# Kernel tuning notes

Hardware: AMD Instinct MI355X
Metric: run time of the kernel (lower is better)

The kernel has to match this reference:

```python
import jax, jax.numpy as jnp
import numpy as np

N_E, E_DIM = 2048, 256
B, H, W = 32, 32, 32


def setup_inputs() -> dict:
    key = jax.random.key(0)
    k1, k2 = jax.random.split(key)
    z = jax.random.normal(k1, (B, E_DIM, H, W), dtype=jnp.float32)
    embedding = jax.random.normal(k2, (N_E, E_DIM), dtype=jnp.float32)
    return {"z": z, "embedding": embedding}


def reference(z, embedding):
    # z: [B, C, H, W] with C == e_dim; embedding: [n_e, e_dim]
    n_e, e_dim = embedding.shape
    b, c, h, w = z.shape
    z_nhwc = jnp.transpose(z, (0, 2, 3, 1))            # [B,H,W,C]
    z_flat = z_nhwc.reshape(-1, e_dim)                 # [L, D]
    # squared euclidean distance: ||z||^2 + ||e||^2 - 2 z.e^T
    d = (
        jnp.sum(z_flat * z_flat, axis=1, keepdims=True)
        + jnp.sum(embedding * embedding, axis=1)
        - 2.0 * jnp.einsum("ld,nd->ln", z_flat, embedding)
    )                                                  # [L, n_e]
    idx = jnp.argmin(d, axis=1)                        # [L]
    z_q = jnp.take(embedding, idx, axis=0).reshape(b, h, w, e_dim)
    # embed_ema=True -> commitment-only loss (codebook updated by EMA, not grads)
    loss = jnp.mean((jax.lax.stop_gradient(z_q) - z_nhwc) ** 2)
    # straight-through estimator
    z_q_st = z_nhwc + jax.lax.stop_gradient(z_q - z_nhwc)
    quantize = jnp.transpose(z_q_st, (0, 3, 1, 2))     # [B,C,H,W]
    # number of distinct codebook entries used (jit-safe via scatter-set)
    used = jnp.sum(jnp.zeros((n_e,), z.dtype).at[idx].set(1.0))
    index = idx.reshape(b, h, w)
    return quantize, loss, index, used
```

## Files before the change

kernel.cpp:

```cpp
#include <hip/hip_runtime.h>
#include <cfloat>

#define Dm 256
#define HW 1024
#define NE 2048
#define L_TOT 32768
#define QOFF 8388608
#define TAU 0.01f

typedef __attribute__((ext_vector_type(8))) short bf16x8;
typedef __attribute__((ext_vector_type(4))) float f32x4;
typedef const __attribute__((address_space(1))) unsigned int* as1_u32p;
typedef __attribute__((address_space(3))) unsigned int* as3_u32p;

#define GLL(gp, lp) __builtin_amdgcn_global_load_lds((as1_u32p)(gp), (as3_u32p)(lp), 16, 0, 0)

__device__ __forceinline__ unsigned short f2bf(float x) {
    unsigned u = __float_as_uint(x);
    unsigned r = (u + 0x7fffu + ((u >> 16) & 1u)) >> 16;
    return (unsigned short)r;
}
__device__ __forceinline__ float bf2f(unsigned short h) {
    return __uint_as_float(((unsigned)h) << 16);
}

__global__ void k_enorm(const float* __restrict__ emb, float* __restrict__ enorm) {
    int w = threadIdx.x >> 6, lane = threadIdx.x & 63;
    int n = blockIdx.x * 4 + w;
    const float4 v = *reinterpret_cast<const float4*>(emb + (size_t)n * Dm + lane * 4);
    double s = (double)v.x * v.x + (double)v.y * v.y + (double)v.z * v.z + (double)v.w * v.w;
    #pragma unroll
    for (int off = 32; off; off >>= 1) s += __shfl_xor(s, off);
    if (lane == 0) enorm[n] = (float)s;
}

__global__ __launch_bounds__(256) void k_split(
    const float* __restrict__ z, const float* __restrict__ emb,
    unsigned short* __restrict__ z_hi, unsigned short* __restrict__ z_lo,
    unsigned short* __restrict__ e_hi, unsigned short* __restrict__ e_lo,
    float* __restrict__ enorm, float* __restrict__ zn_part,
    float* __restrict__ used, int* __restrict__ flag_cnt)
{
    __shared__ unsigned short zh[32][260];
    __shared__ unsigned short zl[32][260];
    __shared__ double zsum[4];
    const int t = threadIdx.x;
    const int w = t >> 6, lane = t & 63;

    if (blockIdx.x >= 16 && blockIdx.x < 24) used[(blockIdx.x - 16) * 256 + t] = 0.f;
    if (blockIdx.x == 24 && t == 0) *flag_cnt = 0;

    if (w < 2) {
        int n = blockIdx.x * 2 + w;
        const float4 v = *reinterpret_cast<const float4*>(emb + (size_t)n * Dm + lane * 4);
        float vv[4] = { v.x, v.y, v.z, v.w };
        double s = (double)v.x * v.x + (double)v.y * v.y + (double)v.z * v.z + (double)v.w * v.w;
        #pragma unroll
        for (int off = 32; off; off >>= 1) s += __shfl_xor(s, off);
        if (lane == 0) enorm[n] = (float)s;
        ushort4 h4, l4;
        unsigned short* hp = (unsigned short*)&h4;
        unsigned short* lp = (unsigned short*)&l4;
        #pragma unroll
        for (int j = 0; j < 4; ++j) {
            unsigned short h = f2bf(vv[j]);
            hp[j] = h;
            lp[j] = f2bf(vv[j] - bf2f(h));
        }
        *reinterpret_cast<ushort4*>(e_hi + (size_t)n * Dm + lane * 4) = h4;
        *reinterpret_cast<ushort4*>(e_lo + (size_t)n * Dm + lane * 4) = l4;
    }

    const int b  = blockIdx.x >> 5;
    const int p0 = (blockIdx.x & 31) * 32;
    const int pp = t & 31, cb = t >> 5;
    const float* zb = z + (size_t)b * (Dm * HW) + p0 + pp;
    float zs = 0.f;
    for (int ci = 0; ci < 32; ++ci) {
        int c = ci * 8 + cb;
        float x = zb[(size_t)c * HW];
        zs = fmaf(x, x, zs);
        unsigned short h = f2bf(x);
        zh[pp][c] = h;
        zl[pp][c] = f2bf(x - bf2f(h));
    }
    double d = zs;
    #pragma unroll
    for (int off = 32; off; off >>= 1) d += __shfl_xor(d, off);
    if ((t & 63) == 0) zsum[w] = d;
    __syncthreads();
    if (t == 0) zn_part[blockIdx.x] = (float)(zsum[0] + zsum[1] + zsum[2] + zsum[3]);
    const int l0 = b * 1024 + p0;
    #pragma unroll
    for (int r = 0; r < 8; ++r) {
        int id = r * 256 + t;
        int row = id >> 6, ch = id & 63;
        *reinterpret_cast<ushort4*>(z_hi + (size_t)(l0 + row) * Dm + ch * 4) =
            *reinterpret_cast<ushort4*>(&zh[row][ch * 4]);
        *reinterpret_cast<ushort4*>(z_lo + (size_t)(l0 + row) * Dm + ch * 4) =
            *reinterpret_cast<ushort4*>(&zl[row][ch * 4]);
    }
}

__global__ __launch_bounds__(512, 4) void k_score2(
    const unsigned short* __restrict__ z_hi, const unsigned short* __restrict__ z_lo,
    const unsigned short* __restrict__ e_hi, const unsigned short* __restrict__ e_lo,
    const float* __restrict__ enorm,
    float* __restrict__ pd1, float* __restrict__ pd2, int* __restrict__ pi1)
{
    __shared__ unsigned short lds[2][2][128 * 64];

    const int t    = threadIdx.x;
    const int lane = t & 63, w = t >> 6;
    const int wm = w >> 2, wn = w & 3;
    const int c15 = lane & 15, g4 = lane >> 4;

    const int bx = blockIdx.x;
    const int wg = (bx & 7) * 64 + (bx >> 3);
    const int mi = wg >> 1, ni = wg & 1;
    const int l0 = mi * 128;
    const int nbase = ni * 1024;

    const int srow = t >> 3;
    const int chg  = (t & 7) ^ (srow & 7);
    const int aoff0 = (l0 + srow) * Dm + chg * 8;
    const int aoff1 = aoff0 + 64 * Dm;
    const int bbase = srow * Dm + chg * 8 + nbase * Dm;
    const int ld0 = t * 8, ld1 = t * 8 + 4096;

    auto stage = [&](int buf, const unsigned short* As, const unsigned short* Bs,
                     int ntoff, int k0) {
        GLL(As + aoff0 + k0,                 &lds[buf][0][ld0]);
        GLL(Bs + bbase + ntoff + k0,         &lds[buf][1][ld0]);
        GLL(As + aoff1 + k0,                 &lds[buf][0][ld1]);
        GLL(Bs + bbase + ntoff + 64 * Dm + k0, &lds[buf][1][ld1]);
    };

    float d1[4][4], d2[4][4]; int i1[4][4];
    #pragma unroll
    for (int m = 0; m < 4; ++m)
        #pragma unroll
        for (int r = 0; r < 4; ++r) { d1[m][r] = 3.4e38f; d2[m][r] = 3.4e38f; i1[m][r] = 0; }

    stage(0, z_hi, e_hi, 0, 0);
    __syncthreads();

    int cur = 0, it = 0;
    int pnt = 0, pkt = 1;
    for (int nt = 0; nt < 8; ++nt) {
        f32x4 acc[4][2];
        #pragma unroll
        for (int m = 0; m < 4; ++m)
            #pragma unroll
            for (int n = 0; n < 2; ++n) acc[m][n] = (f32x4){0.f, 0.f, 0.f, 0.f};

        for (int kt = 0; kt < 12; ++kt, ++it) {
            if (it + 1 < 96) {
                const int nterm = pkt >> 2, nkc = pkt & 3;
                const unsigned short* As = (nterm == 1) ? z_lo : z_hi;
                const unsigned short* Bs = (nterm == 2) ? e_lo : e_hi;
                stage(cur ^ 1, As, Bs, pnt << 15, nkc << 6);
                if (++pkt == 12) { pkt = 0; ++pnt; }
            }
            const unsigned short* Ab = &lds[cur][0][0];
            const unsigned short* Bb = &lds[cur][1][0];
            #pragma unroll
            for (int ks = 0; ks < 2; ++ks) {
                bf16x8 af[4], bfr[2];
                #pragma unroll
                for (int m = 0; m < 4; ++m) {
                    int row = wm * 64 + m * 16 + c15;
                    int cc  = ks * 4 + g4;
                    af[m] = *reinterpret_cast<const bf16x8*>(
                        &Ab[row * 64 + ((cc ^ (row & 7)) << 3)]);
                }
                #pragma unroll
                for (int n = 0; n < 2; ++n) {
                    int row = wn * 32 + n * 16 + c15;
                    int cc  = ks * 4 + g4;
                    bfr[n] = *reinterpret_cast<const bf16x8*>(
                        &Bb[row * 64 + ((cc ^ (row & 7)) << 3)]);
                }
                __builtin_amdgcn_s_setprio(1);
                #pragma unroll
                for (int m = 0; m < 4; ++m)
                    #pragma unroll
                    for (int n = 0; n < 2; ++n)
                        acc[m][n] = __builtin_amdgcn_mfma_f32_16x16x32_bf16(
                            af[m], bfr[n], acc[m][n], 0, 0, 0);
                __builtin_amdgcn_s_setprio(0);
            }
            __syncthreads();
            cur ^= 1;
        }
        int n0 = nbase + nt * 128;
        #pragma unroll
        for (int n = 0; n < 2; ++n) {
            int ng = n0 + wn * 32 + n * 16 + c15;
            float en = enorm[ng];
            #pragma unroll
            for (int m = 0; m < 4; ++m)
                #pragma unroll
                for (int r = 0; r < 4; ++r) {
                    float s = fmaf(-2.f, acc[m][n][r], en);
                    if (s < d1[m][r]) { d2[m][r] = d1[m][r]; d1[m][r] = s; i1[m][r] = ng; }
                    else if (s < d2[m][r]) d2[m][r] = s;
                }
        }
    }

    #pragma unroll
    for (int off = 1; off <= 8; off <<= 1) {
        #pragma unroll
        for (int m = 0; m < 4; ++m)
            #pragma unroll
            for (int r = 0; r < 4; ++r) {
                float od1 = __shfl_xor(d1[m][r], off);
                int   oi1 = __shfl_xor(i1[m][r], off);
                float od2 = __shfl_xor(d2[m][r], off);
                float nd2 = fminf(fminf(d2[m][r], od2), fmaxf(d1[m][r], od1));
                if (od1 < d1[m][r] || (od1 == d1[m][r] && oi1 < i1[m][r])) {
                    d1[m][r] = od1; i1[m][r] = oi1;
                }
                d2[m][r] = nd2;
            }
    }

    float* rs1 = (float*)&lds[0][0][0];
    float* rs2 = rs1 + 3 * 128;
    int*   ri  = (int*)(rs2 + 3 * 128);
    if (wn > 0 && c15 == 0) {
        int s = wn - 1;
        #pragma unroll
        for (int m = 0; m < 4; ++m)
            #pragma unroll
            for (int r = 0; r < 4; ++r) {
                int q = wm * 64 + m * 16 + g4 * 4 + r;
                rs1[s * 128 + q] = d1[m][r];
                rs2[s * 128 + q] = d2[m][r];
                ri [s * 128 + q] = i1[m][r];
            }
    }
    __syncthreads();
    if (wn == 0 && c15 == 0) {
        #pragma unroll
        for (int m = 0; m < 4; ++m)
            #pragma unroll
            for (int r = 0; r < 4; ++r) {
                int q = wm * 64 + m * 16 + g4 * 4 + r;
                float bd1 = d1[m][r], bd2 = d2[m][r]; int bi1 = i1[m][r];
                #pragma unroll
                for (int s = 0; s < 3; ++s) {
                    float od1 = rs1[s * 128 + q], od2 = rs2[s * 128 + q];
                    int   oi1 = ri [s * 128 + q];
                    float nd2 = fminf(fminf(bd2, od2), fmaxf(bd1, od1));
                    if (od1 < bd1 || (od1 == bd1 && oi1 < bi1)) { bd1 = od1; bi1 = oi1; }
                    bd2 = nd2;
                }
                int gq = l0 + q;
                pd1[ni * L_TOT + gq] = bd1;
                pd2[ni * L_TOT + gq] = bd2;
                pi1[ni * L_TOT + gq] = bi1;
            }
    }
}

__global__ __launch_bounds__(256) void k_mg(
    const float* __restrict__ pd1, const float* __restrict__ pd2,
    const int* __restrict__ pi1, const float* __restrict__ emb,
    int* __restrict__ ws_idx, float* __restrict__ out_idxf,
    float* __restrict__ used, int* __restrict__ flag_cnt,
    int* __restrict__ flag_list, float* __restrict__ d1_part,
    float* __restrict__ outq)
{
    __shared__ int sidx[64];
    __shared__ float eldT[Dm][65];
    const int t = threadIdx.x;
    const int l0 = blockIdx.x * 64;
    const int b = l0 >> 10, p0 = l0 & 1023;

    if (t < 64) {
        int gq = l0 + t;
        float d1 = pd1[gq], d2 = pd2[gq]; int i1 = pi1[gq];
        float od1 = pd1[L_TOT + gq], od2 = pd2[L_TOT + gq];
        int   oi1 = pi1[L_TOT + gq];
        float nd2 = fminf(fminf(d2, od2), fmaxf(d1, od1));
        if (od1 < d1 || (od1 == d1 && oi1 < i1)) { d1 = od1; i1 = oi1; }
        d2 = nd2;
        ws_idx[gq] = i1;
        out_idxf[gq] = (float)i1;
        if (d2 - d1 < TAU) {
            int pos = atomicAdd(flag_cnt, 1);
            flag_list[pos] = gq;
        } else {
            used[i1] = 1.0f;
        }
        sidx[t] = i1;
        float s = d1;
        #pragma unroll
        for (int off = 32; off; off >>= 1) s += __shfl_xor(s, off);
        if (t == 0) d1_part[blockIdx.x] = s;
    }
    __syncthreads();

    int w = t >> 6, lane = t & 63;
    for (int r = 0; r < 16; ++r) {
        int q = r * 4 + w;
        const float4 v = *reinterpret_cast<const float4*>(emb + (size_t)sidx[q] * Dm + lane * 4);
        eldT[lane * 4 + 0][q] = v.x; eldT[lane * 4 + 1][q] = v.y;
        eldT[lane * 4 + 2][q] = v.z; eldT[lane * 4 + 3][q] = v.w;
    }
    __syncthreads();
    const size_t obase = (size_t)b * (Dm * HW) + p0 + lane;
    #pragma unroll 4
    for (int it = 0; it < 64; ++it) {
        int c = w * 64 + it;
        outq[obase + (size_t)c * HW] = eldT[c][lane];
    }
}

__global__ __launch_bounds__(256) void k_merge(
    const float* __restrict__ pd1, const float* __restrict__ pd2,
    const int* __restrict__ pi1, int* __restrict__ ws_idx,
    float* __restrict__ out_idxf, float* __restrict__ used,
    int* __restrict__ flag_cnt, int* __restrict__ flag_list,
    float* __restrict__ d1_part)
{
    __shared__ float sdl[256];
    int tt = threadIdx.x;
    int gq = blockIdx.x * 256 + tt;
    float d1 = pd1[gq], d2 = pd2[gq]; int i1 = pi1[gq];
    {
        float od1 = pd1[L_TOT + gq], od2 = pd2[L_TOT + gq];
        int   oi1 = pi1[L_TOT + gq];
        float nd2 = fminf(fminf(d2, od2), fmaxf(d1, od1));
        if (od1 < d1 || (od1 == d1 && oi1 < i1)) { d1 = od1; i1 = oi1; }
        d2 = nd2;
    }
    ws_idx[gq] = i1;
    out_idxf[gq] = (float)i1;
    if (d2 - d1 < TAU) {
        int pos = atomicAdd(flag_cnt, 1);
        flag_list[pos] = gq;
    } else {
        used[i1] = 1.0f;
    }
    sdl[tt] = d1;
    __syncthreads();
    for (int st = 128; st; st >>= 1) {
        if (tt < st) sdl[tt] += sdl[tt + st];
        __syncthreads();
    }
    if (tt == 0) d1_part[blockIdx.x] = sdl[0];
}

#define BM 64
#define BN 128
#define BK 64
__global__ __launch_bounds__(256, 2) void k_argmin_f32(
    const float* __restrict__ z, const float* __restrict__ emb,
    const float* __restrict__ enorm, int* __restrict__ ws_idx,
    float* __restrict__ out_idxf, float* __restrict__ used,
    int* __restrict__ flag_cnt, int* __restrict__ flag_list)
{
    __shared__ float zl[BK][BM];
    __shared__ float el[BK][BN + 4];
    __shared__ float rd1[4][64];
    __shared__ int   ri1[4][64];
    __shared__ float rd2[4][64];

    const int t  = threadIdx.x;
    const int tq = t & 15;
    const int tn = t >> 4;
    const int l0 = blockIdx.x * BM;
    const int b  = l0 >> 10, p0 = l0 & 1023;
    const float* zb = z + (size_t)b * (Dm * HW) + p0;

    float d1[4], d2[4]; int i1[4];
    #pragma unroll
    for (int i = 0; i < 4; ++i) { d1[i] = FLT_MAX; d2[i] = FLT_MAX; i1[i] = 0; }

    for (int nt = 0; nt < NE / BN; ++nt) {
        const int n0 = nt * BN;
        float acc[4][8];
        #pragma unroll
        for (int i = 0; i < 4; ++i)
            #pragma unroll
            for (int j = 0; j < 8; ++j) acc[i][j] = 0.f;

        for (int kc = 0; kc < Dm / BK; ++kc) {
            __syncthreads();
            #pragma unroll
            for (int r = 0; r < 4; ++r) {
                int f = r * 256 + t;
                int kk = f >> 4, q4 = (f & 15) << 2;
                float4 v = *reinterpret_cast<const float4*>(zb + (size_t)(kc * BK + kk) * HW + q4);
                *reinterpret_cast<float4*>(&zl[kk][q4]) = v;
            }
            #pragma unroll
            for (int r = 0; r < 8; ++r) {
                int f = r * 256 + t;
                int n = f >> 4, k4 = (f & 15) << 2;
                float4 v = *reinterpret_cast<const float4*>(emb + (size_t)(n0 + n) * Dm + kc * BK + k4);
                el[k4 + 0][n] = v.x; el[k4 + 1][n] = v.y;
                el[k4 + 2][n] = v.z; el[k4 + 3][n] = v.w;
            }
            __syncthreads();
            #pragma unroll 4
            for (int kk = 0; kk < BK; ++kk) {
                float4 zf = *reinterpret_cast<const float4*>(&zl[kk][tq << 2]);
                float4 e0 = *reinterpret_cast<const float4*>(&el[kk][tn << 3]);
                float4 e1 = *reinterpret_cast<const float4*>(&el[kk][(tn << 3) + 4]);
                float zr[4] = { zf.x, zf.y, zf.z, zf.w };
                float er[8] = { e0.x, e0.y, e0.z, e0.w, e1.x, e1.y, e1.z, e1.w };
                #pragma unroll
                for (int i = 0; i < 4; ++i)
                    #pragma unroll
                    for (int j = 0; j < 8; ++j)
                        acc[i][j] = fmaf(zr[i], er[j], acc[i][j]);
            }
        }
        #pragma unroll
        for (int j = 0; j < 8; ++j) {
            int ng = n0 + (tn << 3) + j;
            float en = enorm[ng];
            #pragma unroll
            for (int i = 0; i < 4; ++i) {
                float s = fmaf(-2.f, acc[i][j], en);
                if (s < d1[i]) { d2[i] = d1[i]; d1[i] = s; i1[i] = ng; }
                else if (s < d2[i]) d2[i] = s;
            }
        }
    }
    #pragma unroll
    for (int off = 16; off <= 32; off <<= 1) {
        #pragma unroll
        for (int i = 0; i < 4; ++i) {
            float od1 = __shfl_xor(d1[i], off);
            int   oi1 = __shfl_xor(i1[i], off);
            float od2 = __shfl_xor(d2[i], off);
            float nd2 = fminf(fminf(d2[i], od2), fmaxf(d1[i], od1));
            bool take = (od1 < d1[i]) || (od1 == d1[i] && oi1 < i1[i]);
            if (take) { d1[i] = od1; i1[i] = oi1; }
            d2[i] = nd2;
        }
    }
    int w = t >> 6;
    if ((t & 63) < 16) {
        #pragma unroll
        for (int i = 0; i < 4; ++i) {
            rd1[w][(tq << 2) + i] = d1[i];
            ri1[w][(tq << 2) + i] = i1[i];
            rd2[w][(tq << 2) + i] = d2[i];
        }
    }
    __syncthreads();
    if (t < 64) {
        float bd1 = rd1[0][t]; int bi1 = ri1[0][t]; float bd2 = rd2[0][t];
        #pragma unroll
        for (int ww = 1; ww < 4; ++ww) {
            float od1 = rd1[ww][t]; int oi1 = ri1[ww][t]; float od2 = rd2[ww][t];
            float nd2 = fminf(fminf(bd2, od2), fmaxf(bd1, od1));
            if (od1 < bd1 || (od1 == bd1 && oi1 < bi1)) { bd1 = od1; bi1 = oi1; }
            bd2 = nd2;
        }
        int l = l0 + t;
        ws_idx[l] = bi1;
        out_idxf[l] = (float)bi1;
        if (bd2 - bd1 < TAU) {
            int pos = atomicAdd(flag_cnt, 1);
            flag_list[pos] = l;
        } else {
            used[bi1] = 1.0f;
        }
    }
}

__global__ void k_refine(const float* __restrict__ z, const float* __restrict__ emb,
                         const int* __restrict__ flag_cnt, const int* __restrict__ flag_list,
                         int* __restrict__ ws_idx, float* __restrict__ out_idxf,
                         float* __restrict__ used, float* __restrict__ outq)
{
    __shared__ float zrow[Dm];
    __shared__ double sd[256];
    __shared__ int    si[256];
    int nf = *flag_cnt;
    for (int fi = blockIdx.x; fi < nf; fi += gridDim.x) {
        int l = flag_list[fi];
        int b = l >> 10, p = l & 1023;
        const float* zq = z + (size_t)b * (Dm * HW) + p;
        __syncthreads();
        for (int c = threadIdx.x; c < Dm; c += blockDim.x) zrow[c] = zq[(size_t)c * HW];
        __syncthreads();
        double bd = DBL_MAX; int bi = 0;
        for (int nb = 0; nb < NE / 256; ++nb) {
            int n = nb * 256 + threadIdx.x;
            const float* er = emb + (size_t)n * Dm;
            double dt0 = 0.0, dt1 = 0.0, dt2 = 0.0, dt3 = 0.0;
            double nm0 = 0.0, nm1 = 0.0, nm2 = 0.0, nm3 = 0.0;
            for (int c = 0; c < Dm; c += 4) {
                double e0 = er[c], e1 = er[c + 1], e2 = er[c + 2], e3 = er[c + 3];
                dt0 += e0 * (double)zrow[c];     nm0 += e0 * e0;
                dt1 += e1 * (double)zrow[c + 1]; nm1 += e1 * e1;
                dt2 += e2 * (double)zrow[c + 2]; nm2 += e2 * e2;
                dt3 += e3 * (double)zrow[c + 3]; nm3 += e3 * e3;
            }
            double s = (nm0 + nm1) + (nm2 + nm3) - 2.0 * ((dt0 + dt1) + (dt2 + dt3));
            if (s < bd) { bd = s; bi = n; }
        }
        sd[threadIdx.x] = bd; si[threadIdx.x] = bi;
        __syncthreads();
        for (int st = 128; st; st >>= 1) {
            if (threadIdx.x < (unsigned)st) {
                double od = sd[threadIdx.x + st]; int oi = si[threadIdx.x + st];
                if (od < sd[threadIdx.x] || (od == sd[threadIdx.x] && oi < si[threadIdx.x])) {
                    sd[threadIdx.x] = od; si[threadIdx.x] = oi;
                }
            }
            __syncthreads();
        }
        if (threadIdx.x == 0) {
            ws_idx[l] = si[0];
            out_idxf[l] = (float)si[0];
            used[si[0]] = 1.0f;
        }
        __syncthreads();
        int bi0 = si[0];
        int c = threadIdx.x;
        outq[(size_t)b * (Dm * HW) + (size_t)c * HW + p] = emb[(size_t)bi0 * Dm + c];
        __syncthreads();
    }
}

__global__ __launch_bounds__(256) void k_gather(
    const float* __restrict__ emb, const int* __restrict__ ws_idx,
    float* __restrict__ outq)
{
    __shared__ int sidx[64];
    __shared__ float eldT[Dm][65];
    const int t = threadIdx.x;
    const int l0 = blockIdx.x * 64;
    const int b = l0 >> 10, p0 = l0 & 1023;
    if (t < 64) sidx[t] = ws_idx[l0 + t];
    __syncthreads();
    int w = t >> 6, lane = t & 63;
    for (int r = 0; r < 16; ++r) {
        int q = r * 4 + w;
        const float4 v = *reinterpret_cast<const float4*>(emb + (size_t)sidx[q] * Dm + lane * 4);
        eldT[lane * 4 + 0][q] = v.x; eldT[lane * 4 + 1][q] = v.y;
        eldT[lane * 4 + 2][q] = v.z; eldT[lane * 4 + 3][q] = v.w;
    }
    __syncthreads();
    const size_t obase = (size_t)b * (Dm * HW) + p0 + lane;
    #pragma unroll 4
    for (int it = 0; it < 64; ++it) {
        int c = w * 64 + it;
        outq[obase + (size_t)c * HW] = eldT[c][lane];
    }
}

__global__ __launch_bounds__(256) void k_gather_loss(
    const float* __restrict__ z, const float* __restrict__ emb,
    const int* __restrict__ ws_idx, float* __restrict__ outq,
    float* __restrict__ partials)
{
    __shared__ int sidx[64];
    __shared__ float eldT[Dm][65];
    __shared__ float wsum[4];
    const int t = threadIdx.x;
    const int l0 = blockIdx.x * 64;
    const int b = l0 >> 10, p0 = l0 & 1023;
    if (t < 64) sidx[t] = ws_idx[l0 + t];
    __syncthreads();
    int w = t >> 6, lane = t & 63;
    for (int r = 0; r < 16; ++r) {
        int q = r * 4 + w;
        const float4 v = *reinterpret_cast<const float4*>(emb + (size_t)sidx[q] * Dm + lane * 4);
        eldT[lane * 4 + 0][q] = v.x; eldT[lane * 4 + 1][q] = v.y;
        eldT[lane * 4 + 2][q] = v.z; eldT[lane * 4 + 3][q] = v.w;
    }
    __syncthreads();
    float ls = 0.f;
    const size_t obase = (size_t)b * (Dm * HW) + p0 + lane;
    for (int it = 0; it < 64; ++it) {
        int c = w * 64 + it;
        size_t o = obase + (size_t)c * HW;
        float qv = eldT[c][lane];
        float zv = z[o];
        outq[o] = qv;
        float df = qv - zv;
        ls = fmaf(df, df, ls);
    }
    #pragma unroll
    for (int off = 32; off; off >>= 1) ls += __shfl_xor(ls, off);
    if (lane == 0) wsum[w] = ls;
    __syncthreads();
    if (t == 0) partials[blockIdx.x] = wsum[0] + wsum[1] + wsum[2] + wsum[3];
}

__global__ void k_final(const float* __restrict__ zn_part, const float* __restrict__ d1_part,
                        int nd1, const float* __restrict__ used,
                        float* __restrict__ out_loss, float* __restrict__ out_used)
{
    __shared__ double s1[256];
    __shared__ float  s2[256];
    int t = threadIdx.x;
    double a = 0.0;
    for (int i = t; i < 1024; i += 256) a += (double)zn_part[i];
    for (int i = t; i < nd1; i += 256) a += (double)d1_part[i];
    float u = 0.f;
    for (int i = t; i < NE; i += 256) u += used[i];
    s1[t] = a; s2[t] = u;
    __syncthreads();
    for (int st = 128; st; st >>= 1) {
        if (t < st) { s1[t] += s1[t + st]; s2[t] += s2[t + st]; }
        __syncthreads();
    }
    if (t == 0) { *out_loss = (float)(s1[0] / 8388608.0); *out_used = s2[0]; }
}

__global__ void k_final_fb(const float* __restrict__ partials, const float* __restrict__ used,
                           float* __restrict__ out_loss, float* __restrict__ out_used)
{
    __shared__ float s1[256], s2[256];
    int t = threadIdx.x;
    float a = partials[t] + partials[t + 256];
    float u = 0.f;
    for (int i = t; i < NE; i += 256) u += used[i];
    s1[t] = a; s2[t] = u;
    __syncthreads();
    for (int st = 128; st; st >>= 1) {
        if (t < st) { s1[t] += s1[t + st]; s2[t] += s2[t + st]; }
        __syncthreads();
    }
    if (t == 0) { *out_loss = s1[0] / 8388608.f; *out_used = s2[0]; }
}

extern "C" void kernel_launch(void* const* d_in, const int* in_sizes, int n_in,
                              void* d_out, int out_size, void* d_ws, size_t ws_size,
                              hipStream_t stream) {
    const float* z   = (const float*)d_in[0];
    const float* emb = (const float*)d_in[1];
    float* out      = (float*)d_out;
    float* outq     = out;
    float* out_loss = out + QOFF;
    float* out_idxf = out + QOFF + 1;
    float* out_used = out + QOFF + 1 + L_TOT;

    float* ws       = (float*)d_ws;
    float* enorm    = ws;
    float* used     = ws + 2048;
    float* zn_part  = ws + 4096;
    float* d1_part  = ws + 5120;
    int*   flag_cnt = (int*)(ws + 5632);
    int*   ws_idx   = (int*)(ws + 5888);
    int*   flag_list= (int*)(ws + 5888 + L_TOT);

    float* pd1w = ws + 71680;
    float* pd2w = ws + 137216;
    int*   pi1w = (int*)(ws + 202752);

    size_t bf_bytes = 2ull * (NE + L_TOT) * Dm * sizeof(unsigned short);
    size_t need_t1 = 268288ull * 4 + bf_bytes;
    size_t need_t2 = 71680ull * 4 + bf_bytes;

    if (ws_size >= need_t1) {
        unsigned short* e_hi = (unsigned short*)(ws + 268288);
        unsigned short* e_lo = e_hi + (size_t)NE * Dm;
        unsigned short* z_hi = e_lo + (size_t)NE * Dm;
        unsigned short* z_lo = z_hi + (size_t)L_TOT * Dm;
        k_split<<<1024, 256, 0, stream>>>(z, emb, z_hi, z_lo, e_hi, e_lo,
                                          enorm, zn_part, used, flag_cnt);
        k_score2<<<512, 512, 0, stream>>>(z_hi, z_lo, e_hi, e_lo, enorm, pd1w, pd2w, pi1w);
        k_mg<<<L_TOT / 64, 256, 0, stream>>>(pd1w, pd2w, pi1w, emb, ws_idx, out_idxf,
                                             used, flag_cnt, flag_list, d1_part, outq);
        k_refine<<<256, 256, 0, stream>>>(z, emb, flag_cnt, flag_list, ws_idx, out_idxf,
                                          used, outq);
        k_final<<<1, 256, 0, stream>>>(zn_part, d1_part, 512, used, out_loss, out_used);
    } else if (ws_size >= need_t2) {
        unsigned short* e_hi = (unsigned short*)(ws + 71680);
        unsigned short* e_lo = e_hi + (size_t)NE * Dm;
        unsigned short* z_hi = e_lo + (size_t)NE * Dm;
        unsigned short* z_lo = z_hi + (size_t)L_TOT * Dm;
        float* pd1 = outq;
        float* pd2 = outq + 2 * L_TOT;
        int*   pi1 = (int*)(outq + 4 * L_TOT);
        k_split<<<1024, 256, 0, stream>>>(z, emb, z_hi, z_lo, e_hi, e_lo,
                                          enorm, zn_part, used, flag_cnt);
        k_score2<<<512, 512, 0, stream>>>(z_hi, z_lo, e_hi, e_lo, enorm, pd1, pd2, pi1);
        k_merge<<<L_TOT / 256, 256, 0, stream>>>(pd1, pd2, pi1, ws_idx, out_idxf, used,
                                                 flag_cnt, flag_list, d1_part);
        k_refine<<<256, 256, 0, stream>>>(z, emb, flag_cnt, flag_list, ws_idx, out_idxf,
                                          used, outq);
        k_gather<<<L_TOT / 64, 256, 0, stream>>>(emb, ws_idx, outq);
        k_final<<<1, 256, 0, stream>>>(zn_part, d1_part, 128, used, out_loss, out_used);
    } else {
        hipMemsetAsync(used, 0, (size_t)3584 * 4, stream);
        k_enorm<<<NE / 4, 256, 0, stream>>>(emb, enorm);
        k_argmin_f32<<<L_TOT / BM, 256, 0, stream>>>(z, emb, enorm, ws_idx, out_idxf, used,
                                                     flag_cnt, flag_list);
        k_refine<<<256, 256, 0, stream>>>(z, emb, flag_cnt, flag_list, ws_idx, out_idxf,
                                          used, outq);
        k_gather_loss<<<L_TOT / 64, 256, 0, stream>>>(z, emb, ws_idx, outq, zn_part);
        k_final_fb<<<1, 256, 0, stream>>>(zn_part, used, out_loss, out_used);
    }
}
```

Measured before the change: 235.0 us.

## Use 4-wave blocks with 64x64 per-wave tiles in score GEMM

Moves the score kernel from 8 waves per block, each computing a 64x32 sub-tile, to 4 waves per block, each computing a 64x64 sub-tile. The block tile stays 128x128, so each thread now issues twice the staging loads. The aim is to raise MFMA work per LDS fragment load (register-level reuse of A fragments) and to shrink the cross-wave argmin merge from four partners to two. The cost is twice the accumulator registers per thread and fewer resident waves to hide latency.

New measurement: 232.5 us. Within noise of the previous version (-1.0%).

```diff
diff --git a/kernel.cpp b/kernel.cpp
--- a/kernel.cpp
+++ b/kernel.cpp
@@ -102,7 +102,7 @@
     }
 }
 
-__global__ __launch_bounds__(512, 4) void k_score2(
+__global__ __launch_bounds__(256, 2) void k_score3(
     const unsigned short* __restrict__ z_hi, const unsigned short* __restrict__ z_lo,
     const unsigned short* __restrict__ e_hi, const unsigned short* __restrict__ e_lo,
     const float* __restrict__ enorm,
@@ -112,7 +112,7 @@
 
     const int t    = threadIdx.x;
     const int lane = t & 63, w = t >> 6;
-    const int wm = w >> 2, wn = w & 3;
+    const int wm = w >> 1, wc = w & 1;
     const int c15 = lane & 15, g4 = lane >> 4;
 
     const int bx = blockIdx.x;
@@ -124,16 +124,19 @@
     const int srow = t >> 3;
     const int chg  = (t & 7) ^ (srow & 7);
     const int aoff0 = (l0 + srow) * Dm + chg * 8;
-    const int aoff1 = aoff0 + 64 * Dm;
-    const int bbase = srow * Dm + chg * 8 + nbase * Dm;
-    const int ld0 = t * 8, ld1 = t * 8 + 4096;
+    const int bbas0 = srow * Dm + chg * 8 + nbase * Dm;
+    const int ld0 = t * 8;
 
     auto stage = [&](int buf, const unsigned short* As, const unsigned short* Bs,
                      int ntoff, int k0) {
-        GLL(As + aoff0 + k0,                 &lds[buf][0][ld0]);
-        GLL(Bs + bbase + ntoff + k0,         &lds[buf][1][ld0]);
-        GLL(As + aoff1 + k0,                 &lds[buf][0][ld1]);
-        GLL(Bs + bbase + ntoff + 64 * Dm + k0, &lds[buf][1][ld1]);
+        GLL(As + aoff0 + k0,                   &lds[buf][0][ld0]);
+        GLL(Bs + bbas0 + ntoff + k0,           &lds[buf][1][ld0]);
+        GLL(As + aoff0 + 32 * Dm + k0,         &lds[buf][0][ld0 + 2048]);
+        GLL(Bs + bbas0 + ntoff + 32 * Dm + k0, &lds[buf][1][ld0 + 2048]);
+        GLL(As + aoff0 + 64 * Dm + k0,         &lds[buf][0][ld0 + 4096]);
+        GLL(Bs + bbas0 + ntoff + 64 * Dm + k0, &lds[buf][1][ld0 + 4096]);
+        GLL(As + aoff0 + 96 * Dm + k0,         &lds[buf][0][ld0 + 6144]);
+        GLL(Bs + bbas0 + ntoff + 96 * Dm + k0, &lds[buf][1][ld0 + 6144]);
     };
 
     float d1[4][4], d2[4][4]; int i1[4][4];
@@ -148,11 +151,11 @@
     int cur = 0, it = 0;
     int pnt = 0, pkt = 1;
     for (int nt = 0; nt < 8; ++nt) {
-        f32x4 acc[4][2];
+        f32x4 acc[4][4];
         #pragma unroll
         for (int m = 0; m < 4; ++m)
             #pragma unroll
-            for (int n = 0; n < 2; ++n) acc[m][n] = (f32x4){0.f, 0.f, 0.f, 0.f};
+            for (int n = 0; n < 4; ++n) acc[m][n] = (f32x4){0.f, 0.f, 0.f, 0.f};
 
         for (int kt = 0; kt < 12; ++kt, ++it) {
             if (it + 1 < 96) {
@@ -166,7 +169,7 @@
             const unsigned short* Bb = &lds[cur][1][0];
             #pragma unroll
             for (int ks = 0; ks < 2; ++ks) {
-                bf16x8 af[4], bfr[2];
+                bf16x8 af[4], bfr[4];
                 #pragma unroll
                 for (int m = 0; m < 4; ++m) {
                     int row = wm * 64 + m * 16 + c15;
@@ -175,8 +178,8 @@
                         &Ab[row * 64 + ((cc ^ (row & 7)) << 3)]);
                 }
                 #pragma unroll
-                for (int n = 0; n < 2; ++n) {
-                    int row = wn * 32 + n * 16 + c15;
+                for (int n = 0; n < 4; ++n) {
+                    int row = wc * 64 + n * 16 + c15;
                     int cc  = ks * 4 + g4;
                     bfr[n] = *reinterpret_cast<const bf16x8*>(
                         &Bb[row * 64 + ((cc ^ (row & 7)) << 3)]);
@@ -185,7 +188,7 @@
                 #pragma unroll
                 for (int m = 0; m < 4; ++m)
                     #pragma unroll
-                    for (int n = 0; n < 2; ++n)
+                    for (int n = 0; n < 4; ++n)
                         acc[m][n] = __builtin_amdgcn_mfma_f32_16x16x32_bf16(
                             af[m], bfr[n], acc[m][n], 0, 0, 0);
                 __builtin_amdgcn_s_setprio(0);
@@ -195,8 +198,8 @@
         }
         int n0 = nbase + nt * 128;
         #pragma unroll
-        for (int n = 0; n < 2; ++n) {
-            int ng = n0 + wn * 32 + n * 16 + c15;
+        for (int n = 0; n < 4; ++n) {
+            int ng = n0 + wc * 64 + n * 16 + c15;
             float en = enorm[ng];
             #pragma unroll
             for (int m = 0; m < 4; ++m)
@@ -227,36 +230,32 @@
     }
 
     float* rs1 = (float*)&lds[0][0][0];
-    float* rs2 = rs1 + 3 * 128;
-    int*   ri  = (int*)(rs2 + 3 * 128);
-    if (wn > 0 && c15 == 0) {
-        int s = wn - 1;
+    float* rs2 = rs1 + 128;
+    int*   ri  = (int*)(rs2 + 128);
+    if (wc == 1 && c15 == 0) {
         #pragma unroll
         for (int m = 0; m < 4; ++m)
             #pragma unroll
             for (int r = 0; r < 4; ++r) {
                 int q = wm * 64 + m * 16 + g4 * 4 + r;
-                rs1[s * 128 + q] = d1[m][r];
-                rs2[s * 128 + q] = d2[m][r];
-                ri [s * 128 + q] = i1[m][r];
-            }
-    }
-    __syncthreads();
-    if (wn == 0 && c15 == 0) {
+                rs1[q] = d1[m][r];
+                rs2[q] = d2[m][r];
+                ri [q] = i1[m][r];
+            }
+    }
+    __syncthreads();
+    if (wc == 0 && c15 == 0) {
         #pragma unroll
         for (int m = 0; m < 4; ++m)
             #pragma unroll
             for (int r = 0; r < 4; ++r) {
                 int q = wm * 64 + m * 16 + g4 * 4 + r;
                 float bd1 = d1[m][r], bd2 = d2[m][r]; int bi1 = i1[m][r];
-                #pragma unroll
-                for (int s = 0; s < 3; ++s) {
-                    float od1 = rs1[s * 128 + q], od2 = rs2[s * 128 + q];
-                    int   oi1 = ri [s * 128 + q];
-                    float nd2 = fminf(fminf(bd2, od2), fmaxf(bd1, od1));
-                    if (od1 < bd1 || (od1 == bd1 && oi1 < bi1)) { bd1 = od1; bi1 = oi1; }
-                    bd2 = nd2;
-                }
+                float od1 = rs1[q], od2 = rs2[q];
+                int   oi1 = ri [q];
+                float nd2 = fminf(fminf(bd2, od2), fmaxf(bd1, od1));
+                if (od1 < bd1 || (od1 == bd1 && oi1 < bi1)) { bd1 = od1; bi1 = oi1; }
+                bd2 = nd2;
                 int gq = l0 + q;
                 pd1[ni * L_TOT + gq] = bd1;
                 pd2[ni * L_TOT + gq] = bd2;
@@ -671,7 +670,7 @@
         unsigned short* z_lo = z_hi + (size_t)L_TOT * Dm;
         k_split<<<1024, 256, 0, stream>>>(z, emb, z_hi, z_lo, e_hi, e_lo,
                                           enorm, zn_part, used, flag_cnt);
-        k_score2<<<512, 512, 0, stream>>>(z_hi, z_lo, e_hi, e_lo, enorm, pd1w, pd2w, pi1w);
+        k_score3<<<512, 256, 0, stream>>>(z_hi, z_lo, e_hi, e_lo, enorm, pd1w, pd2w, pi1w);
         k_mg<<<L_TOT / 64, 256, 0, stream>>>(pd1w, pd2w, pi1w, emb, ws_idx, out_idxf,
                                              used, flag_cnt, flag_list, d1_part, outq);
         k_refine<<<256, 256, 0, stream>>>(z, emb, flag_cnt, flag_list, ws_idx, out_idxf,
@@ -687,7 +686,7 @@
         int*   pi1 = (int*)(outq + 4 * L_TOT);
         k_split<<<1024, 256, 0, stream>>>(z, emb, z_hi, z_lo, e_hi, e_lo,
                                           enorm, zn_part, used, flag_cnt);
-        k_score2<<<512, 512, 0, stream>>>(z_hi, z_lo, e_hi, e_lo, enorm, pd1, pd2, pi1);
+        k_score3<<<512, 256, 0, stream>>>(z_hi, z_lo, e_hi, e_lo, enorm, pd1, pd2, pi1);
         k_merge<<<L_TOT / 256, 256, 0, stream>>>(pd1, pd2, pi1, ws_idx, out_idxf, used,
                                                  flag_cnt, flag_list, d1_part);
         k_refine<<<256, 256, 0, stream>>>(z, emb, flag_cnt, flag_list, ws_idx, out_idxf,
```
